# Kernel optimization log

Measured on AMD Instinct MI355X. Metric: run time of the kernel, lower is better.

The kernel has to match this reference:

```python
import jax, jax.numpy as jnp
import numpy as np

N = 50000    # nodes
E = 800000   # edges
F = 128      # node_feature_dim
H = 128      # GCN hidden
H2 = 64      # fc1 hidden
T = 8        # num_tactics
G = 64       # graphs in batch


def setup_inputs() -> dict:
    key = jax.random.key(0)
    ks = jax.random.split(key, 12)
    s = 0.05
    return {
        "x": jax.random.normal(ks[0], (N, F), jnp.float32),
        "edge_index": jax.random.randint(ks[1], (2, E), 0, N, dtype=jnp.int32),
        "batch": jnp.sort(jax.random.randint(ks[2], (N,), 0, G, dtype=jnp.int32)),
        "W": jax.random.normal(ks[3], (F, H), jnp.float32) * s,
        "b": jax.random.normal(ks[4], (H,), jnp.float32) * s,
        "fc1_w": jax.random.normal(ks[5], (H, H2), jnp.float32) * s,
        "fc1_b": jax.random.normal(ks[6], (H2,), jnp.float32) * s,
        "actor_w": jax.random.normal(ks[7], (H2, T), jnp.float32) * s,
        "actor_b": jax.random.normal(ks[8], (T,), jnp.float32) * s,
        "critic_w": jax.random.normal(ks[9], (H2, 1), jnp.float32) * s,
        "critic_b": jax.random.normal(ks[10], (1,), jnp.float32) * s,
    }


def _gcn_conv(x, edge_index, W, b):
    # PyG GCNConv: add self-loops, symmetric D^-1/2 (A+I) D^-1/2 normalization,
    # linear transform first, then scatter-add aggregation, then bias.
    n = x.shape[0]
    loops = jnp.arange(n, dtype=edge_index.dtype)
    src = jnp.concatenate([edge_index[0], loops])  # message sources (x_j)
    dst = jnp.concatenate([edge_index[1], loops])  # aggregation targets
    deg = jax.ops.segment_sum(jnp.ones_like(dst, jnp.float32), dst, num_segments=N)
    dinv = deg ** -0.5  # deg >= 1 due to self-loops
    norm = dinv[src] * dinv[dst]                   # [E+N]
    h = x @ W                                      # [N, H]
    msgs = h[src] * norm[:, None]                  # [E+N, H]
    return jax.ops.segment_sum(msgs, dst, num_segments=N) + b


def reference(x, edge_index, batch, W, b, fc1_w, fc1_b, actor_w, actor_b, critic_w, critic_b):
    h = jax.nn.relu(_gcn_conv(x, edge_index, W, b))            # [N, H]
    # global_mean_pool over batch index
    sums = jax.ops.segment_sum(h, batch, num_segments=G)       # [G, H]
    cnts = jax.ops.segment_sum(jnp.ones((h.shape[0],), h.dtype), batch, num_segments=G)
    group_state = sums / jnp.maximum(cnts, 1.0)[:, None]
    z = jax.nn.relu(group_state @ fc1_w + fc1_b)               # [G, H2]
    tactic_probs = jax.nn.softmax(z @ actor_w + actor_b, axis=-1)  # [G, T]
    group_value = z @ critic_w + critic_b                      # [G, 1]
    return tactic_probs, group_value
```

## Files before the change

### kernel.cpp

```cpp
#include <hip/hip_runtime.h>
#include <hip/hip_bf16.h>

#define NN 50000
#define EE 800000
#define FF 128
#define HH 128
#define HID2 64
#define TT 8
#define GG 64
#define NB 196
#define NSB 256
#define EPB (EE / NSB)
#define NPAD 50048

using frag_ab = __attribute__((ext_vector_type(8))) short;
using frag_cd = __attribute__((ext_vector_type(4))) float;

__device__ inline unsigned short f2bf(float f) {
    union { float f; unsigned u; } v; v.f = f;
    unsigned r = v.u + 0x7fff + ((v.u >> 16) & 1);
    return (unsigned short)(r >> 16);
}

__global__ __launch_bounds__(256) void k_front(const int* __restrict__ dst,
                                               const float* __restrict__ W,
                                               int* __restrict__ table,
                                               unsigned short* __restrict__ wt_bf,
                                               float* __restrict__ gsum) {
    __shared__ int cnt[NB];
    int t = threadIdx.x, blk = blockIdx.x;
    if (blk < 64) {
        int gid = blk * 256 + t;
        int c = gid >> 7, k = gid & 127;
        wt_bf[gid] = f2bf(W[k * 128 + c]);
    }
    if (blk >= 64 && blk < 96) {
        int gid = (blk - 64) * 256 + t;
        gsum[gid] = 0.f;
    }
    for (int i = t; i < NB; i += 256) cnt[i] = 0;
    __syncthreads();
    int e0 = blk * EPB;
    for (int e = e0 + t; e < e0 + EPB; e += 256)
        atomicAdd(&cnt[dst[e] >> 8], 1);
    __syncthreads();
    for (int i = t; i < NB; i += 256) table[blk * NB + i] = cnt[i];
}

__global__ __launch_bounds__(256) void kb2a(int* __restrict__ table,
                                            int* __restrict__ ctot) {
    __shared__ int s[256];
    int t = threadIdx.x, b = blockIdx.x;
    int v = table[t * NB + b];
    s[t] = v;
    __syncthreads();
    for (int off = 1; off < 256; off <<= 1) {
        int a = s[t];
        int w = (t >= off) ? s[t - off] : 0;
        __syncthreads();
        s[t] = a + w;
        __syncthreads();
    }
    table[t * NB + b] = s[t] - v;
    if (t == 255) ctot[b] = s[255];
}

__global__ __launch_bounds__(256) void kb2b(const int* __restrict__ ctot,
                                            int* __restrict__ bbase) {
    __shared__ int s[256];
    int b = threadIdx.x;
    int v = (b < NB) ? ctot[b] : 0;
    s[b] = v;
    __syncthreads();
    for (int off = 1; off < 256; off <<= 1) {
        int a = s[b];
        int w = (b >= off) ? s[b - off] : 0;
        __syncthreads();
        s[b] = a + w;
        __syncthreads();
    }
    if (b < NB) bbase[b] = s[b] - v;
    if (b == 0) bbase[NB] = EE;
}

__global__ __launch_bounds__(256) void kb3(const int* __restrict__ src,
                                           const int* __restrict__ dst,
                                           const int* __restrict__ table,
                                           const int* __restrict__ bbase,
                                           unsigned* __restrict__ etmp) {
    __shared__ int ofs[NB];
    __shared__ int cur[NB];
    int t = threadIdx.x, blk = blockIdx.x;
    for (int i = t; i < NB; i += 256) {
        ofs[i] = table[blk * NB + i] + bbase[i];
        cur[i] = 0;
    }
    __syncthreads();
    int e0 = blk * EPB;
    for (int e = e0 + t; e < e0 + EPB; e += 256) {
        int d = dst[e];
        int b = d >> 8;
        int r = atomicAdd(&cur[b], 1);
        etmp[ofs[b] + r] = ((unsigned)d << 16) | (unsigned)src[e];
    }
}

__global__ __launch_bounds__(256) void k_csr(const unsigned* __restrict__ etmp,
                                             const int* __restrict__ bbase,
                                             int* __restrict__ row_ptr,
                                             float* __restrict__ dinv,
                                             int* __restrict__ srcs) {
    __shared__ int s[256];
    __shared__ int cur[256];
    int t = threadIdx.x, b = blockIdx.x;
    s[t] = 0;
    __syncthreads();
    int e0 = bbase[b], e1 = bbase[b + 1];
    for (int e = e0 + t; e < e1; e += 256)
        atomicAdd(&s[(etmp[e] >> 16) & 255], 1);
    __syncthreads();
    int v = s[t];
    for (int off = 1; off < 256; off <<= 1) {
        int a = s[t];
        int w = (t >= off) ? s[t - off] : 0;
        __syncthreads();
        s[t] = a + w;
        __syncthreads();
    }
    int excl = s[t] - v + e0;
    int node = b * 256 + t;
    if (node < NN) {
        row_ptr[node] = excl;
        dinv[node] = rsqrtf((float)(v + 1));
    }
    if (b == NB - 1 && t == 0) row_ptr[NN] = EE;
    cur[t] = excl;
    __syncthreads();
    for (int e = e0 + t; e < e1; e += 256) {
        unsigned u = etmp[e];
        int slot = atomicAdd(&cur[(u >> 16) & 255], 1);
        srcs[slot] = (int)(u & 0xffffu);
    }
}

__global__ __launch_bounds__(256) void k_gemm(const float* __restrict__ x,
                                              const unsigned short* __restrict__ wt_bf,
                                              const float* __restrict__ dinv,
                                              unsigned short* __restrict__ hs) {
    int tid = threadIdx.x;
    int w = tid >> 6, lane = tid & 63;
    int m = lane & 15, quad = lane >> 4;
    int r0 = blockIdx.x * 64 + w * 16;
    int row = r0 + m;
    frag_cd acc[8];
#pragma unroll
    for (int nt = 0; nt < 8; nt++) acc[nt] = frag_cd{0.f, 0.f, 0.f, 0.f};

#pragma unroll
    for (int k0 = 0; k0 < 128; k0 += 32) {
        unsigned short av[8];
        if (row < NN) {
            const float4* p = (const float4*)(x + (size_t)row * 128 + k0 + quad * 8);
            float4 a0 = p[0], a1 = p[1];
            av[0] = f2bf(a0.x); av[1] = f2bf(a0.y); av[2] = f2bf(a0.z); av[3] = f2bf(a0.w);
            av[4] = f2bf(a1.x); av[5] = f2bf(a1.y); av[6] = f2bf(a1.z); av[7] = f2bf(a1.w);
        } else {
#pragma unroll
            for (int j = 0; j < 8; j++) av[j] = 0;
        }
        frag_ab a = *(const frag_ab*)av;
#pragma unroll
        for (int nt = 0; nt < 8; nt++) {
            frag_ab bfr = *(const frag_ab*)(wt_bf + (size_t)(nt * 16 + m) * 128 + k0 + quad * 8);
            acc[nt] = __builtin_amdgcn_mfma_f32_16x16x32_bf16(a, bfr, acc[nt], 0, 0, 0);
        }
    }
#pragma unroll
    for (int reg = 0; reg < 4; reg++) {
        int gr = r0 + quad * 4 + reg;
        if (gr < NN) {
            float di = dinv[gr];
#pragma unroll
            for (int nt = 0; nt < 8; nt++)
                hs[(size_t)gr * 128 + nt * 16 + m] = f2bf(acc[nt][reg] * di);
        }
    }
}

#define ACC8(u) \
    a0 += __uint_as_float((u).x << 16); a1 += __uint_as_float((u).x & 0xffff0000u); \
    a2 += __uint_as_float((u).y << 16); a3 += __uint_as_float((u).y & 0xffff0000u); \
    a4 += __uint_as_float((u).z << 16); a5 += __uint_as_float((u).z & 0xffff0000u); \
    a6 += __uint_as_float((u).w << 16); a7 += __uint_as_float((u).w & 0xffff0000u);

__global__ __launch_bounds__(256) void k_aggr(const uint4* __restrict__ hs4,
                                              const int* __restrict__ row_ptr,
                                              const int* __restrict__ srcs,
                                              const float* __restrict__ dinv,
                                              const float* __restrict__ bias,
                                              const int* __restrict__ batch,
                                              float* __restrict__ gsum) {
    __shared__ float gacc[8 * 128];
    int tid = threadIdx.x;
    int qid = tid >> 4, sub = tid & 15;
    int i_base = blockIdx.x * 32;
    int g_first = batch[i_base];
    int last = i_base + 31; if (last >= NN) last = NN - 1;
    int gspan = batch[last] - g_first + 1;
    bool lds_pool = (gspan <= 8);
    int slots = lds_pool ? gspan : 0;
    for (int idx = tid; idx < slots * 128; idx += 256) gacc[idx] = 0.f;
    __syncthreads();

    const float4* b4 = (const float4*)(bias + sub * 8);
    float4 bb0 = b4[0], bb1 = b4[1];

    float racc[8];
#pragma unroll
    for (int j = 0; j < 8; j++) racc[j] = 0.f;
    int cur_lg = -1;

    for (int n = 0; n < 2; n++) {
        int i = i_base + qid * 2 + n;
        if (i >= NN) break;
        int lg = batch[i] - g_first;
        if (lg != cur_lg) {
            if (cur_lg >= 0) {
                float* gp = lds_pool ? &gacc[cur_lg * 128 + sub * 8]
                                     : &gsum[(g_first + cur_lg) * 128 + sub * 8];
#pragma unroll
                for (int j = 0; j < 8; j++) atomicAdd(&gp[j], racc[j]);
#pragma unroll
                for (int j = 0; j < 8; j++) racc[j] = 0.f;
            }
            cur_lg = lg;
        }
        float di = dinv[i];
        uint4 su = hs4[(size_t)i * 16 + sub];
        float a0 = __uint_as_float(su.x << 16);
        float a1 = __uint_as_float(su.x & 0xffff0000u);
        float a2 = __uint_as_float(su.y << 16);
        float a3 = __uint_as_float(su.y & 0xffff0000u);
        float a4 = __uint_as_float(su.z << 16);
        float a5 = __uint_as_float(su.z & 0xffff0000u);
        float a6 = __uint_as_float(su.w << 16);
        float a7 = __uint_as_float(su.w & 0xffff0000u);
        int e = row_ptr[i], e1 = row_ptr[i + 1];
        for (; e + 7 < e1; e += 8) {
            int s0 = srcs[e],     s1 = srcs[e + 1], s2 = srcs[e + 2], s3 = srcs[e + 3];
            int s4 = srcs[e + 4], s5 = srcs[e + 5], s6 = srcs[e + 6], s7 = srcs[e + 7];
            uint4 u0 = hs4[(size_t)s0 * 16 + sub];
            uint4 u1 = hs4[(size_t)s1 * 16 + sub];
            uint4 u2 = hs4[(size_t)s2 * 16 + sub];
            uint4 u3 = hs4[(size_t)s3 * 16 + sub];
            uint4 u4 = hs4[(size_t)s4 * 16 + sub];
            uint4 u5 = hs4[(size_t)s5 * 16 + sub];
            uint4 u6 = hs4[(size_t)s6 * 16 + sub];
            uint4 u7 = hs4[(size_t)s7 * 16 + sub];
            ACC8(u0) ACC8(u1) ACC8(u2) ACC8(u3)
            ACC8(u4) ACC8(u5) ACC8(u6) ACC8(u7)
        }
        for (; e + 3 < e1; e += 4) {
            int s0 = srcs[e], s1 = srcs[e + 1], s2 = srcs[e + 2], s3 = srcs[e + 3];
            uint4 u0 = hs4[(size_t)s0 * 16 + sub];
            uint4 u1 = hs4[(size_t)s1 * 16 + sub];
            uint4 u2 = hs4[(size_t)s2 * 16 + sub];
            uint4 u3 = hs4[(size_t)s3 * 16 + sub];
            ACC8(u0) ACC8(u1) ACC8(u2) ACC8(u3)
        }
        for (; e < e1; ++e) {
            uint4 u0 = hs4[(size_t)srcs[e] * 16 + sub];
            ACC8(u0)
        }
        racc[0] += fmaxf(fmaf(a0, di, bb0.x), 0.f);
        racc[1] += fmaxf(fmaf(a1, di, bb0.y), 0.f);
        racc[2] += fmaxf(fmaf(a2, di, bb0.z), 0.f);
        racc[3] += fmaxf(fmaf(a3, di, bb0.w), 0.f);
        racc[4] += fmaxf(fmaf(a4, di, bb1.x), 0.f);
        racc[5] += fmaxf(fmaf(a5, di, bb1.y), 0.f);
        racc[6] += fmaxf(fmaf(a6, di, bb1.z), 0.f);
        racc[7] += fmaxf(fmaf(a7, di, bb1.w), 0.f);
    }
    if (cur_lg >= 0) {
        float* gp = lds_pool ? &gacc[cur_lg * 128 + sub * 8]
                             : &gsum[(g_first + cur_lg) * 128 + sub * 8];
#pragma unroll
        for (int j = 0; j < 8; j++) atomicAdd(&gp[j], racc[j]);
    }
    __syncthreads();
    for (int idx = tid; idx < slots * 128; idx += 256) {
        float v = gacc[idx];
        if (v != 0.f)
            atomicAdd(&gsum[(g_first + (idx >> 7)) * 128 + (idx & 127)], v);
    }
}

__device__ inline int lbound(const int* __restrict__ a, int n, int key) {
    int lo = 0, hi = n;
    while (lo < hi) {
        int mid = (lo + hi) >> 1;
        if (a[mid] < key) lo = mid + 1;
        else hi = mid;
    }
    return lo;
}

__global__ __launch_bounds__(64) void k_head(const float* __restrict__ gsum,
                                             const int* __restrict__ batch,
                                             const float* __restrict__ fc1_w,
                                             const float* __restrict__ fc1_b,
                                             const float* __restrict__ actor_w,
                                             const float* __restrict__ actor_b,
                                             const float* __restrict__ critic_w,
                                             const float* __restrict__ critic_b,
                                             float* __restrict__ out) {
    __shared__ float gs[128];
    __shared__ float zs[64];
    __shared__ float ls[8], es[8];
    int g = blockIdx.x, t = threadIdx.x;
    int lo = lbound(batch, NN, g), hi = lbound(batch, NN, g + 1);
    float invc = 1.f / fmaxf((float)(hi - lo), 1.f);
    gs[t] = gsum[g * 128 + t] * invc;
    gs[t + 64] = gsum[g * 128 + 64 + t] * invc;
    __syncthreads();
    float z = fc1_b[t];
    for (int k = 0; k < 128; k++) z = fmaf(gs[k], fc1_w[k * 64 + t], z);
    zs[t] = fmaxf(z, 0.f);
    __syncthreads();
    if (t < 8) {
        float l = actor_b[t];
        for (int k = 0; k < 64; k++) l = fmaf(zs[k], actor_w[k * 8 + t], l);
        ls[t] = l;
    }
    __syncthreads();
    if (t < 8) {
        float m = ls[0];
#pragma unroll
        for (int j = 1; j < 8; j++) m = fmaxf(m, ls[j]);
        es[t] = expf(ls[t] - m);
    }
    __syncthreads();
    if (t < 8) {
        float ssum = 0.f;
#pragma unroll
        for (int j = 0; j < 8; j++) ssum += es[j];
        out[g * 8 + t] = es[t] / ssum;
    }
    if (t == 32) {
        float v = critic_b[0];
        for (int k = 0; k < 64; k++) v = fmaf(zs[k], critic_w[k], v);
        out[GG * TT + g] = v;
    }
}

extern "C" void kernel_launch(void* const* d_in, const int* in_sizes, int n_in,
                              void* d_out, int out_size, void* d_ws, size_t ws_size,
                              hipStream_t stream) {
    const float* x        = (const float*)d_in[0];
    const int*   ei       = (const int*)d_in[1];
    const int*   batch    = (const int*)d_in[2];
    const float* W        = (const float*)d_in[3];
    const float* b        = (const float*)d_in[4];
    const float* fc1_w    = (const float*)d_in[5];
    const float* fc1_b    = (const float*)d_in[6];
    const float* actor_w  = (const float*)d_in[7];
    const float* actor_b  = (const float*)d_in[8];
    const float* critic_w = (const float*)d_in[9];
    const float* critic_b = (const float*)d_in[10];
    float* out = (float*)d_out;

    char* ws = (char*)d_ws;
    size_t off = 0;
    unsigned short* hs    = (unsigned short*)(ws + off); off += (size_t)NN * 128 * 2 + 64;
    unsigned short* wt_bf = (unsigned short*)(ws + off); off += (size_t)128 * 128 * 2;
    float* dinv      = (float*)(ws + off);    off += (size_t)NN * 4;
    int*   row_ptr   = (int*)(ws + off);      off += (size_t)(NN + 1) * 4 + 12;
    int*   srcs      = (int*)(ws + off);      off += (size_t)EE * 4;
    unsigned* etmp   = (unsigned*)(ws + off); off += (size_t)EE * 4;
    int*   table     = (int*)(ws + off);      off += (size_t)NSB * NB * 4;
    int*   bbase     = (int*)(ws + off);      off += (size_t)(NB + 1) * 4 + 12;
    int*   ctot      = (int*)(ws + off);      off += (size_t)NB * 4 + 16;
    float* gsum      = (float*)(ws + off);    off += (size_t)GG * HH * 4;

    const int* src = ei;
    const int* dst = ei + EE;

    k_front<<<NSB, 256, 0, stream>>>(dst, W, table, wt_bf, gsum);
    kb2a<<<NB, 256, 0, stream>>>(table, ctot);
    kb2b<<<1, 256, 0, stream>>>(ctot, bbase);
    kb3<<<NSB, 256, 0, stream>>>(src, dst, table, bbase, etmp);
    k_csr<<<NB, 256, 0, stream>>>(etmp, bbase, row_ptr, dinv, srcs);
    k_gemm<<<NPAD / 64, 256, 0, stream>>>(x, wt_bf, dinv, hs);
    k_aggr<<<(NN + 31) / 32, 256, 0, stream>>>((const uint4*)hs, row_ptr, srcs,
                                               dinv, b, batch, gsum);
    k_head<<<GG, 64, 0, stream>>>(gsum, batch, fc1_w, fc1_b, actor_w, actor_b,
                                  critic_w, critic_b, out);
}
```

Measured before the change: 194.7 us.

## Merge scan and scatter kernels, co-launch GEMM, apply source dinv in aggregation

The two prefix-scan kernels and the scatter kernel are folded into one kernel. Each block recomputes its column prefix directly from the count table, which removes two launches and the ctot buffer. The GEMM blocks are appended to the same grid so the feature transform runs alongside edge bucketing, which means it can no longer depend on dinv. The source-side normalisation therefore moves into aggregation as an extra gathered dinv[src] load plus an FMA per edge. That saves launches and overlaps work, but adds redundant table reads in every scatter block and extra random loads in the gather loop.

New measurement: 188.1 us. 3.4% less time.

```diff
diff --git a/kernel.cpp b/kernel.cpp
--- a/kernel.cpp
+++ b/kernel.cpp
@@ -12,6 +12,7 @@
 #define NSB 256
 #define EPB (EE / NSB)
 #define NPAD 50048
+#define GEMMB (NPAD / 64)
 
 using frag_ab = __attribute__((ext_vector_type(8))) short;
 using frag_cd = __attribute__((ext_vector_type(4))) float;
@@ -20,6 +21,16 @@
     union { float f; unsigned u; } v; v.f = f;
     unsigned r = v.u + 0x7fff + ((v.u >> 16) & 1);
     return (unsigned short)(r >> 16);
+}
+
+__device__ inline int lbound(const int* __restrict__ a, int n, int key) {
+    int lo = 0, hi = n;
+    while (lo < hi) {
+        int mid = (lo + hi) >> 1;
+        if (a[mid] < key) lo = mid + 1;
+        else hi = mid;
+    }
+    return lo;
 }
 
 __global__ __launch_bounds__(256) void k_front(const int* __restrict__ dst,
@@ -47,61 +58,89 @@
     for (int i = t; i < NB; i += 256) table[blk * NB + i] = cnt[i];
 }
 
-__global__ __launch_bounds__(256) void kb2a(int* __restrict__ table,
-                                            int* __restrict__ ctot) {
-    __shared__ int s[256];
-    int t = threadIdx.x, b = blockIdx.x;
-    int v = table[t * NB + b];
-    s[t] = v;
-    __syncthreads();
-    for (int off = 1; off < 256; off <<= 1) {
-        int a = s[t];
-        int w = (t >= off) ? s[t - off] : 0;
+__global__ __launch_bounds__(256) void k_sg(const int* __restrict__ src,
+                                            const int* __restrict__ dst,
+                                            const int* __restrict__ table,
+                                            int* __restrict__ bbase,
+                                            unsigned* __restrict__ etmp,
+                                            const float* __restrict__ x,
+                                            const unsigned short* __restrict__ wt_bf,
+                                            unsigned short* __restrict__ hs) {
+    int t = threadIdx.x, blk = blockIdx.x;
+    if (blk < NSB) {
+        __shared__ int s[256];
+        __shared__ int ofs[NB];
+        __shared__ int cur[NB];
+        int pr = 0, to = 0;
+        if (t < NB) {
+#pragma unroll 8
+            for (int r = 0; r < 256; r++) {
+                int v = table[r * NB + t];
+                to += v;
+                pr += (r < blk) ? v : 0;
+            }
+        }
+        s[t] = (t < NB) ? to : 0;
         __syncthreads();
-        s[t] = a + w;
+        for (int off = 1; off < 256; off <<= 1) {
+            int a = s[t];
+            int w = (t >= off) ? s[t - off] : 0;
+            __syncthreads();
+            s[t] = a + w;
+            __syncthreads();
+        }
+        if (t < NB) {
+            int bb = s[t] - to;
+            ofs[t] = pr + bb;
+            cur[t] = 0;
+            if (blk == 0) bbase[t] = bb;
+        }
+        if (blk == 0 && t == 0) bbase[NB] = EE;
         __syncthreads();
-    }
-    table[t * NB + b] = s[t] - v;
-    if (t == 255) ctot[b] = s[255];
-}
-
-__global__ __launch_bounds__(256) void kb2b(const int* __restrict__ ctot,
-                                            int* __restrict__ bbase) {
-    __shared__ int s[256];
-    int b = threadIdx.x;
-    int v = (b < NB) ? ctot[b] : 0;
-    s[b] = v;
-    __syncthreads();
-    for (int off = 1; off < 256; off <<= 1) {
-        int a = s[b];
-        int w = (b >= off) ? s[b - off] : 0;
-        __syncthreads();
-        s[b] = a + w;
-        __syncthreads();
-    }
-    if (b < NB) bbase[b] = s[b] - v;
-    if (b == 0) bbase[NB] = EE;
-}
-
-__global__ __launch_bounds__(256) void kb3(const int* __restrict__ src,
-                                           const int* __restrict__ dst,
-                                           const int* __restrict__ table,
-                                           const int* __restrict__ bbase,
-                                           unsigned* __restrict__ etmp) {
-    __shared__ int ofs[NB];
-    __shared__ int cur[NB];
-    int t = threadIdx.x, blk = blockIdx.x;
-    for (int i = t; i < NB; i += 256) {
-        ofs[i] = table[blk * NB + i] + bbase[i];
-        cur[i] = 0;
-    }
-    __syncthreads();
-    int e0 = blk * EPB;
-    for (int e = e0 + t; e < e0 + EPB; e += 256) {
-        int d = dst[e];
-        int b = d >> 8;
-        int r = atomicAdd(&cur[b], 1);
-        etmp[ofs[b] + r] = ((unsigned)d << 16) | (unsigned)src[e];
+        int e0 = blk * EPB;
+        for (int e = e0 + t; e < e0 + EPB; e += 256) {
+            int d = dst[e];
+            int b = d >> 8;
+            int r = atomicAdd(&cur[b], 1);
+            etmp[ofs[b] + r] = ((unsigned)d << 16) | (unsigned)src[e];
+        }
+    } else {
+        int vb = blk - NSB;
+        int w = t >> 6, lane = t & 63;
+        int m = lane & 15, quad = lane >> 4;
+        int r0 = vb * 64 + w * 16;
+        int row = r0 + m;
+        frag_cd acc[8];
+#pragma unroll
+        for (int nt = 0; nt < 8; nt++) acc[nt] = frag_cd{0.f, 0.f, 0.f, 0.f};
+#pragma unroll
+        for (int k0 = 0; k0 < 128; k0 += 32) {
+            unsigned short av[8];
+            if (row < NN) {
+                const float4* pp = (const float4*)(x + (size_t)row * 128 + k0 + quad * 8);
+                float4 a0 = pp[0], a1 = pp[1];
+                av[0] = f2bf(a0.x); av[1] = f2bf(a0.y); av[2] = f2bf(a0.z); av[3] = f2bf(a0.w);
+                av[4] = f2bf(a1.x); av[5] = f2bf(a1.y); av[6] = f2bf(a1.z); av[7] = f2bf(a1.w);
+            } else {
+#pragma unroll
+                for (int j = 0; j < 8; j++) av[j] = 0;
+            }
+            frag_ab a = *(const frag_ab*)av;
+#pragma unroll
+            for (int nt = 0; nt < 8; nt++) {
+                frag_ab bfr = *(const frag_ab*)(wt_bf + (size_t)(nt * 16 + m) * 128 + k0 + quad * 8);
+                acc[nt] = __builtin_amdgcn_mfma_f32_16x16x32_bf16(a, bfr, acc[nt], 0, 0, 0);
+            }
+        }
+#pragma unroll
+        for (int reg = 0; reg < 4; reg++) {
+            int gr = r0 + quad * 4 + reg;
+            if (gr < NN) {
+#pragma unroll
+                for (int nt = 0; nt < 8; nt++)
+                    hs[(size_t)gr * 128 + nt * 16 + m] = f2bf(acc[nt][reg]);
+            }
+        }
     }
 }
 
@@ -143,55 +182,15 @@
     }
 }
 
-__global__ __launch_bounds__(256) void k_gemm(const float* __restrict__ x,
-                                              const unsigned short* __restrict__ wt_bf,
-                                              const float* __restrict__ dinv,
-                                              unsigned short* __restrict__ hs) {
-    int tid = threadIdx.x;
-    int w = tid >> 6, lane = tid & 63;
-    int m = lane & 15, quad = lane >> 4;
-    int r0 = blockIdx.x * 64 + w * 16;
-    int row = r0 + m;
-    frag_cd acc[8];
-#pragma unroll
-    for (int nt = 0; nt < 8; nt++) acc[nt] = frag_cd{0.f, 0.f, 0.f, 0.f};
-
-#pragma unroll
-    for (int k0 = 0; k0 < 128; k0 += 32) {
-        unsigned short av[8];
-        if (row < NN) {
-            const float4* p = (const float4*)(x + (size_t)row * 128 + k0 + quad * 8);
-            float4 a0 = p[0], a1 = p[1];
-            av[0] = f2bf(a0.x); av[1] = f2bf(a0.y); av[2] = f2bf(a0.z); av[3] = f2bf(a0.w);
-            av[4] = f2bf(a1.x); av[5] = f2bf(a1.y); av[6] = f2bf(a1.z); av[7] = f2bf(a1.w);
-        } else {
-#pragma unroll
-            for (int j = 0; j < 8; j++) av[j] = 0;
-        }
-        frag_ab a = *(const frag_ab*)av;
-#pragma unroll
-        for (int nt = 0; nt < 8; nt++) {
-            frag_ab bfr = *(const frag_ab*)(wt_bf + (size_t)(nt * 16 + m) * 128 + k0 + quad * 8);
-            acc[nt] = __builtin_amdgcn_mfma_f32_16x16x32_bf16(a, bfr, acc[nt], 0, 0, 0);
-        }
-    }
-#pragma unroll
-    for (int reg = 0; reg < 4; reg++) {
-        int gr = r0 + quad * 4 + reg;
-        if (gr < NN) {
-            float di = dinv[gr];
-#pragma unroll
-            for (int nt = 0; nt < 8; nt++)
-                hs[(size_t)gr * 128 + nt * 16 + m] = f2bf(acc[nt][reg] * di);
-        }
-    }
-}
-
-#define ACC8(u) \
-    a0 += __uint_as_float((u).x << 16); a1 += __uint_as_float((u).x & 0xffff0000u); \
-    a2 += __uint_as_float((u).y << 16); a3 += __uint_as_float((u).y & 0xffff0000u); \
-    a4 += __uint_as_float((u).z << 16); a5 += __uint_as_float((u).z & 0xffff0000u); \
-    a6 += __uint_as_float((u).w << 16); a7 += __uint_as_float((u).w & 0xffff0000u);
+#define ACCS(u, ds) \
+    a0 = fmaf(ds, __uint_as_float((u).x << 16), a0); \
+    a1 = fmaf(ds, __uint_as_float((u).x & 0xffff0000u), a1); \
+    a2 = fmaf(ds, __uint_as_float((u).y << 16), a2); \
+    a3 = fmaf(ds, __uint_as_float((u).y & 0xffff0000u), a3); \
+    a4 = fmaf(ds, __uint_as_float((u).z << 16), a4); \
+    a5 = fmaf(ds, __uint_as_float((u).z & 0xffff0000u), a5); \
+    a6 = fmaf(ds, __uint_as_float((u).w << 16), a6); \
+    a7 = fmaf(ds, __uint_as_float((u).w & 0xffff0000u), a7);
 
 __global__ __launch_bounds__(256) void k_aggr(const uint4* __restrict__ hs4,
                                               const int* __restrict__ row_ptr,
@@ -237,18 +236,20 @@
         }
         float di = dinv[i];
         uint4 su = hs4[(size_t)i * 16 + sub];
-        float a0 = __uint_as_float(su.x << 16);
-        float a1 = __uint_as_float(su.x & 0xffff0000u);
-        float a2 = __uint_as_float(su.y << 16);
-        float a3 = __uint_as_float(su.y & 0xffff0000u);
-        float a4 = __uint_as_float(su.z << 16);
-        float a5 = __uint_as_float(su.z & 0xffff0000u);
-        float a6 = __uint_as_float(su.w << 16);
-        float a7 = __uint_as_float(su.w & 0xffff0000u);
+        float a0 = di * __uint_as_float(su.x << 16);
+        float a1 = di * __uint_as_float(su.x & 0xffff0000u);
+        float a2 = di * __uint_as_float(su.y << 16);
+        float a3 = di * __uint_as_float(su.y & 0xffff0000u);
+        float a4 = di * __uint_as_float(su.z << 16);
+        float a5 = di * __uint_as_float(su.z & 0xffff0000u);
+        float a6 = di * __uint_as_float(su.w << 16);
+        float a7 = di * __uint_as_float(su.w & 0xffff0000u);
         int e = row_ptr[i], e1 = row_ptr[i + 1];
         for (; e + 7 < e1; e += 8) {
             int s0 = srcs[e],     s1 = srcs[e + 1], s2 = srcs[e + 2], s3 = srcs[e + 3];
             int s4 = srcs[e + 4], s5 = srcs[e + 5], s6 = srcs[e + 6], s7 = srcs[e + 7];
+            float d0 = dinv[s0], d1 = dinv[s1], d2 = dinv[s2], d3 = dinv[s3];
+            float d4 = dinv[s4], d5 = dinv[s5], d6 = dinv[s6], d7 = dinv[s7];
             uint4 u0 = hs4[(size_t)s0 * 16 + sub];
             uint4 u1 = hs4[(size_t)s1 * 16 + sub];
             uint4 u2 = hs4[(size_t)s2 * 16 + sub];
@@ -257,20 +258,23 @@
             uint4 u5 = hs4[(size_t)s5 * 16 + sub];
             uint4 u6 = hs4[(size_t)s6 * 16 + sub];
             uint4 u7 = hs4[(size_t)s7 * 16 + sub];
-            ACC8(u0) ACC8(u1) ACC8(u2) ACC8(u3)
-            ACC8(u4) ACC8(u5) ACC8(u6) ACC8(u7)
+            ACCS(u0, d0) ACCS(u1, d1) ACCS(u2, d2) ACCS(u3, d3)
+            ACCS(u4, d4) ACCS(u5, d5) ACCS(u6, d6) ACCS(u7, d7)
         }
         for (; e + 3 < e1; e += 4) {
             int s0 = srcs[e], s1 = srcs[e + 1], s2 = srcs[e + 2], s3 = srcs[e + 3];
+            float d0 = dinv[s0], d1 = dinv[s1], d2 = dinv[s2], d3 = dinv[s3];
             uint4 u0 = hs4[(size_t)s0 * 16 + sub];
             uint4 u1 = hs4[(size_t)s1 * 16 + sub];
             uint4 u2 = hs4[(size_t)s2 * 16 + sub];
             uint4 u3 = hs4[(size_t)s3 * 16 + sub];
-            ACC8(u0) ACC8(u1) ACC8(u2) ACC8(u3)
+            ACCS(u0, d0) ACCS(u1, d1) ACCS(u2, d2) ACCS(u3, d3)
         }
         for (; e < e1; ++e) {
-            uint4 u0 = hs4[(size_t)srcs[e] * 16 + sub];
-            ACC8(u0)
+            int s0 = srcs[e];
+            float d0 = dinv[s0];
+            uint4 u0 = hs4[(size_t)s0 * 16 + sub];
+            ACCS(u0, d0)
         }
         racc[0] += fmaxf(fmaf(a0, di, bb0.x), 0.f);
         racc[1] += fmaxf(fmaf(a1, di, bb0.y), 0.f);
@@ -293,16 +297,6 @@
         if (v != 0.f)
             atomicAdd(&gsum[(g_first + (idx >> 7)) * 128 + (idx & 127)], v);
     }
-}
-
-__device__ inline int lbound(const int* __restrict__ a, int n, int key) {
-    int lo = 0, hi = n;
-    while (lo < hi) {
-        int mid = (lo + hi) >> 1;
-        if (a[mid] < key) lo = mid + 1;
-        else hi = mid;
-    }
-    return lo;
 }
 
 __global__ __launch_bounds__(64) void k_head(const float* __restrict__ gsum,
@@ -379,18 +373,15 @@
     unsigned* etmp   = (unsigned*)(ws + off); off += (size_t)EE * 4;
     int*   table     = (int*)(ws + off);      off += (size_t)NSB * NB * 4;
     int*   bbase     = (int*)(ws + off);      off += (size_t)(NB + 1) * 4 + 12;
-    int*   ctot      = (int*)(ws + off);      off += (size_t)NB * 4 + 16;
     float* gsum      = (float*)(ws + off);    off += (size_t)GG * HH * 4;
 
     const int* src = ei;
     const int* dst = ei + EE;
 
     k_front<<<NSB, 256, 0, stream>>>(dst, W, table, wt_bf, gsum);
-    kb2a<<<NB, 256, 0, stream>>>(table, ctot);
-    kb2b<<<1, 256, 0, stream>>>(ctot, bbase);
-    kb3<<<NSB, 256, 0, stream>>>(src, dst, table, bbase, etmp);
+    k_sg<<<NSB + GEMMB, 256, 0, stream>>>(src, dst, table, bbase, etmp,
+                                          x, wt_bf, hs);
     k_csr<<<NB, 256, 0, stream>>>(etmp, bbase, row_ptr, dinv, srcs);
-    k_gemm<<<NPAD / 64, 256, 0, stream>>>(x, wt_bf, dinv, hs);
     k_aggr<<<(NN + 31) / 32, 256, 0, stream>>>((const uint4*)hs, row_ptr, srcs,
                                                dinv, b, batch, gsum);
     k_head<<<GG, 64, 0, stream>>>(gsum, batch, fc1_w, fc1_b, actor_w, actor_b,
```
